# Kernel optimization log

Measured on AMD Instinct MI355X. Metric: run time of the kernel, lower is better.

Reference implementation:

```python
import jax, jax.numpy as jnp
import numpy as np

N = 100000   # nodes
E = 800000   # edges
IN = 128     # in_channels == embedding_size (required by residual Linear)
EMB = 128
OUT = 64
EPS = 1e-5   # GraphNorm eps (PyG default)


def setup_inputs() -> dict:
    key = jax.random.key(0)
    ks = jax.random.split(key, 8)
    x = jax.random.normal(ks[0], (N, IN), jnp.float32)
    edge_index = jax.random.randint(ks[1], (2, E), 0, N, dtype=jnp.int64)
    g = lambda k, shape, scale: jax.random.normal(k, shape, jnp.float32) * scale
    return dict(
        x=x,
        edge_index=edge_index,
        W1=g(ks[2], (IN, EMB), IN ** -0.5), b1=jnp.zeros((EMB,), jnp.float32),
        W2=g(ks[3], (EMB, EMB), EMB ** -0.5), b2=jnp.zeros((EMB,), jnp.float32),
        gn1_w=1.0 + g(ks[4], (EMB,), 0.05), gn1_b=jnp.zeros((EMB,), jnp.float32), gn1_ms=jnp.ones((EMB,), jnp.float32),
        gn2_w=1.0 + g(ks[5], (EMB,), 0.05), gn2_b=jnp.zeros((EMB,), jnp.float32), gn2_ms=jnp.ones((EMB,), jnp.float32),
        Wr=g(ks[6], (EMB, OUT), EMB ** -0.5), br=jnp.zeros((OUT,), jnp.float32),
    )


def _gcn_conv(x, W, b, src, dst, dinv):
    # PyG GCNConv: h = x @ W; out[i] = sum_{(j->i)} dinv[j]*dinv[i]*h[j]; out += bias
    h = x @ W
    norm = (dinv[src] * dinv[dst])[:, None]        # [E+N, 1]
    msg = h[src] * norm                             # gather + scale (irregular)
    out = jax.ops.segment_sum(msg, dst, num_segments=N)  # scatter-add
    return out + b


def _graph_norm(h, w, b, ms):
    # PyG GraphNorm, single graph: mean/var over node dim
    mean = jnp.mean(h, axis=0)
    c = h - ms * mean
    var = jnp.mean(c * c, axis=0)
    return w * c * jax.lax.rsqrt(var + EPS) + b


def reference(x, edge_index, W1, b1, W2, b2, gn1_w, gn1_b, gn1_ms, gn2_w, gn2_b, gn2_ms, Wr, br):
    loops = jnp.arange(N, dtype=edge_index.dtype)
    src = jnp.concatenate([edge_index[0], loops])   # add self-loops
    dst = jnp.concatenate([edge_index[1], loops])
    deg = jax.ops.segment_sum(jnp.ones_like(src, dtype=x.dtype), dst, num_segments=N)
    dinv = jnp.where(deg > 0, jax.lax.rsqrt(jnp.maximum(deg, 1.0)), 0.0)

    # dropout is identity in eval mode
    x1 = jax.nn.relu(_graph_norm(_gcn_conv(x, W1, b1, src, dst, dinv), gn1_w, gn1_b, gn1_ms))
    x2 = jax.nn.relu(_graph_norm(_gcn_conv(x1, W2, b2, src, dst, dinv), gn2_w, gn2_b, gn2_ms))
    return (x1 + x2) @ Wr + br
```

## Files before the change

kernel.cpp:

```cpp
#include <hip/hip_runtime.h>
#include <hip/hip_bf16.h>

typedef __attribute__((ext_vector_type(8))) short bf16x8;
typedef __attribute__((ext_vector_type(4))) float f32x4;
typedef __attribute__((ext_vector_type(2))) float f32x2;
typedef __attribute__((ext_vector_type(4))) unsigned int u32x4;

#define STATS_BLOCKS 256
#define SLOTS 32

__device__ __forceinline__ int coh_load(const int* p){
  return __hip_atomic_load(p, __ATOMIC_RELAXED, __HIP_MEMORY_SCOPE_AGENT);
}
__device__ __forceinline__ unsigned int coh_loadu(const unsigned int* p){
  return __hip_atomic_load(p, __ATOMIC_RELAXED, __HIP_MEMORY_SCOPE_AGENT);
}

__device__ __forceinline__ float bf2f(unsigned short u){
  union { unsigned int i; float f; } v; v.i = ((unsigned int)u) << 16; return v.f;
}
__device__ __forceinline__ unsigned short f2bf(float f){
  union { float f; unsigned int i; } v; v.f = f;
  return (unsigned short)((v.i + 0x7fffu + ((v.i >> 16) & 1u)) >> 16);
}
__device__ __forceinline__ f32x2 bf2x(unsigned int w){
  union { unsigned int i; float f; } lo, hi;
  lo.i = w << 16; hi.i = w & 0xffff0000u;
  f32x2 r; r.x = lo.f; r.y = hi.f; return r;
}


__global__ __launch_bounds__(256) void k_setup(
    const float* __restrict__ W1, const float* __restrict__ W2, const float* __restrict__ Wr,
    unsigned short* __restrict__ wp1, unsigned short* __restrict__ wp2,
    unsigned short* __restrict__ wpr,
    const int* __restrict__ dst, int* __restrict__ hist, int E, int NBUK){
  int b = blockIdx.x;
  if (b < 160){
    int pb = b;
    const float* W; unsigned short* wp; int ncols;
    if (pb < 64)      { W = W1; wp = wp1; ncols = 128; }
    else if (pb < 128){ W = W2; wp = wp2; ncols = 128; pb -= 64; }
    else              { W = Wr; wp = wpr; ncols = 64;  pb -= 128; }
    int idx = pb*256 + threadIdx.x;
    if (idx >= 128*ncols) return;
    int bb = idx & 7, lane = (idx>>3)&63, kk = (idx>>9)&3, ct = idx>>11;
    int k = kk*32 + ((lane>>4)<<3) + bb;
    int c = ct*16 + (lane&15);
    wp[idx] = f2bf(W[k*ncols + c]);
    return;
  }
  int c = b - 160;
  __shared__ int hcnt[256];
  hcnt[threadIdx.x] = 0;
  __syncthreads();
  int per = (E + 255) >> 8;
  int e0 = c*per, e1 = min(E, e0 + per);
  for (int e = e0 + threadIdx.x; e < e1; e += 256)
    atomicAdd(&hcnt[dst[e] >> 9], 1);
  __syncthreads();
  int t = threadIdx.x;
  if (t < NBUK) hist[t*256 + c] = hcnt[t];
}


__global__ __launch_bounds__(256) void k_scanA(int* __restrict__ hist,
                                               int* __restrict__ btot){
  int b = blockIdx.x, t = threadIdx.x;
  int v = hist[b*256 + t];
  __shared__ int sh[256];
  sh[t] = v; __syncthreads();
  for (int o = 1; o < 256; o <<= 1){
    int x = (t >= o) ? sh[t-o] : 0;
    __syncthreads();
    sh[t] += x;
    __syncthreads();
  }
  hist[b*256 + t] = sh[t] - v;
  if (t == 255) btot[b] = sh[255];
}


__global__ __launch_bounds__(256) void k_scanB(const int* __restrict__ btot,
                                               int* __restrict__ bstart, int NBUK){
  int t = threadIdx.x;
  int v = (t < NBUK) ? btot[t] : 0;
  __shared__ int sh[256];
  sh[t] = v; __syncthreads();
  for (int o = 1; o < 256; o <<= 1){
    int x = (t >= o) ? sh[t-o] : 0;
    __syncthreads();
    sh[t] += x;
    __syncthreads();
  }
  if (t < NBUK){
    bstart[t] = sh[t] - v;
    if (t == NBUK-1) bstart[NBUK] = sh[t];
  }
}


__global__ __launch_bounds__(256) void k_scatter(const int* __restrict__ src,
    const int* __restrict__ dst, const int* __restrict__ hist,
    const int* __restrict__ bstart, unsigned int* __restrict__ ebuf, int E, int NBUK){
  __shared__ int cursor[256];
  int c = blockIdx.x, t = threadIdx.x;
  if (t < NBUK) cursor[t] = hist[t*256 + c] + bstart[t];
  __syncthreads();
  int per = (E + 255) >> 8;
  int e0 = c*per, e1 = min(E, e0 + per);
  for (int e = e0 + t; e < e1; e += 256){
    int d = dst[e], s = src[e];
    int bin = d >> 9;
    int pos = atomicAdd(&cursor[bin], 1);
    ebuf[pos] = ((unsigned int)(d & 511) << 17) | (unsigned int)s;
  }
}


__global__ __launch_bounds__(256) void k_bucket(const unsigned int* __restrict__ ebuf,
    const int* __restrict__ bstart, int* __restrict__ cur, int* __restrict__ col, int N){
  __shared__ int cnt[512];
  int b = blockIdx.x, t = threadIdx.x;
  cnt[t] = 0; cnt[t + 256] = 0;
  __syncthreads();
  int e0 = bstart[b], e1 = bstart[b+1];
  int base = b << 9;
  for (int e = e0 + t; e < e1; e += 256){
    unsigned int v = coh_loadu(&ebuf[e]);
    int dl = (int)(v >> 17);
    int s  = (int)(v & 0x1FFFFu);
    int p = atomicAdd(&cnt[dl], 1);
    if (p < SLOTS) col[(size_t)(base + dl)*SLOTS + p] = s;
  }
  __syncthreads();
  int d0 = base + t, d1 = base + t + 256;
  if (d0 < N) cur[d0] = cnt[t];
  if (d1 < N) cur[d1] = cnt[t + 256];
}


__global__ __launch_bounds__(256) void k_gemm1(const float* __restrict__ A,
    const unsigned short* __restrict__ wp, const int* cur,
    unsigned short* __restrict__ h, int nTiles){
  int gw = (int)((blockIdx.x*256 + threadIdx.x) >> 6);
  if (gw >= nTiles) return;
  int lane = threadIdx.x & 63;
  int row0 = gw*16;
  int r  = row0 + (lane & 15);
  int kb = (lane >> 4) * 8;
  bf16x8 a[4];
#pragma unroll
  for (int kk = 0; kk < 4; ++kk){
    const float* p = A + (size_t)r*128 + kk*32 + kb;
    f32x4 v0 = *reinterpret_cast<const f32x4*>(p);
    f32x4 v1 = *reinterpret_cast<const f32x4*>(p + 4);
#pragma unroll
    for (int b = 0; b < 4; ++b){ a[kk][b] = (short)f2bf(v0[b]); a[kk][4+b] = (short)f2bf(v1[b]); }
  }
  int cst = lane & 15;
  int rb  = row0 + ((lane >> 4) << 2);
  float dv[4];
#pragma unroll
  for (int b2 = 0; b2 < 4; ++b2) dv[b2] = rsqrtf(1.0f + (float)coh_load(&cur[rb + b2]));
#pragma unroll
  for (int ct = 0; ct < 8; ++ct){
    f32x4 acc = {0.f,0.f,0.f,0.f};
#pragma unroll
    for (int kk = 0; kk < 4; ++kk){
      bf16x8 b = *reinterpret_cast<const bf16x8*>(wp + ((ct*4 + kk)*64 + lane)*8);
      acc = __builtin_amdgcn_mfma_f32_16x16x32_bf16(a[kk], b, acc, 0, 0, 0);
    }
    int c = ct*16 + cst;
#pragma unroll
    for (int b2 = 0; b2 < 4; ++b2)
      h[(size_t)(rb + b2)*128 + c] = f2bf(dv[b2]*acc[b2]);
  }
}


__global__ __launch_bounds__(256) void k_agg(const unsigned short* __restrict__ h,
    const int* cur, const int* col,
    const float* __restrict__ bias, unsigned short* __restrict__ agg, int N){
  int i = (int)((blockIdx.x*256 + threadIdx.x) >> 6);
  if (i >= N) return;
  int lane = threadIdx.x & 63;
  int q  = lane >> 4;
  int cl = lane & 15;
  const u32x4* hp = reinterpret_cast<const u32x4*>(h);
  int craw = coh_load(&cur[i]);
  int colv = coh_load(&col[i*SLOTS + min(lane, SLOTS-1)]);
  int c = min(craw, SLOTS);
  int idx = (lane < c) ? colv : i;
  f32x2 a0 = {0.f,0.f}, a1 = {0.f,0.f}, a2 = {0.f,0.f}, a3 = {0.f,0.f};
  int j = 0;
  for (; j + 8 <= c; j += 8){
    int r0 = __shfl(idx, j + q);
    int r1 = __shfl(idx, j + 4 + q);
    u32x4 v0 = hp[(size_t)r0*16 + cl];
    u32x4 v1 = hp[(size_t)r1*16 + cl];
    a0 += bf2x(v0.x) + bf2x(v1.x);
    a1 += bf2x(v0.y) + bf2x(v1.y);
    a2 += bf2x(v0.z) + bf2x(v1.z);
    a3 += bf2x(v0.w) + bf2x(v1.w);
  }
  int rem = c - j;
  if (rem > 0){
    int r0 = __shfl(idx, j + q);
    int r1 = __shfl(idx, j + 4 + q);
    if (q < rem){
      u32x4 v0 = hp[(size_t)r0*16 + cl];
      a0 += bf2x(v0.x); a1 += bf2x(v0.y); a2 += bf2x(v0.z); a3 += bf2x(v0.w);
    }
    if (q + 4 < rem){
      u32x4 v1 = hp[(size_t)r1*16 + cl];
      a0 += bf2x(v1.x); a1 += bf2x(v1.y); a2 += bf2x(v1.z); a3 += bf2x(v1.w);
    }
  }
  float acc[8] = {a0.x, a0.y, a1.x, a1.y, a2.x, a2.y, a3.x, a3.y};
#pragma unroll
  for (int b = 0; b < 8; ++b){
    acc[b] += __shfl_xor(acc[b], 16);
    acc[b] += __shfl_xor(acc[b], 32);
  }
  if (q == 0){
    u32x4 hv = hp[(size_t)i*16 + cl];
    float di = rsqrtf(1.0f + (float)craw);
    f32x2 s0 = bf2x(hv.x), s1 = bf2x(hv.y), s2 = bf2x(hv.z), s3 = bf2x(hv.w);
    float sf[8] = {s0.x, s0.y, s1.x, s1.y, s2.x, s2.y, s3.x, s3.y};
    unsigned short o[8];
#pragma unroll
    for (int b = 0; b < 8; ++b)
      o[b] = f2bf(di*(acc[b] + sf[b]) + bias[cl*8 + b]);
    u32x4 ov;
    ov.x = (unsigned int)o[0] | ((unsigned int)o[1] << 16);
    ov.y = (unsigned int)o[2] | ((unsigned int)o[3] << 16);
    ov.z = (unsigned int)o[4] | ((unsigned int)o[5] << 16);
    ov.w = (unsigned int)o[6] | ((unsigned int)o[7] << 16);
    reinterpret_cast<u32x4*>(agg)[(size_t)i*16 + cl] = ov;
  }
}


__global__ __launch_bounds__(256) void k_stats(const unsigned short* __restrict__ agg,
    float* __restrict__ partials, int N){
  int tid = blockIdx.x*256 + threadIdx.x;
  int g = threadIdx.x & 15;
  int c0 = g * 8;
  float S1[8] = {0,0,0,0,0,0,0,0}, S2[8] = {0,0,0,0,0,0,0,0};
  size_t total = (size_t)N * 16;
  for (size_t p = tid; p < total; p += (size_t)STATS_BLOCKS*256){
    bf16x8 v = reinterpret_cast<const bf16x8*>(agg)[p];
#pragma unroll
    for (int b = 0; b < 8; ++b){
      float f = bf2f((unsigned short)v[b]);
      S1[b] += f; S2[b] += f*f;
    }
  }
  __shared__ float sh1[16][128];
  __shared__ float sh2[16][128];
  int cp = threadIdx.x >> 4;
#pragma unroll
  for (int b = 0; b < 8; ++b){ sh1[cp][c0 + b] = S1[b]; sh2[cp][c0 + b] = S2[b]; }
  __syncthreads();
  int t = threadIdx.x;
  if (t < 128){
    float s = 0.f;
#pragma unroll
    for (int qq = 0; qq < 16; ++qq) s += sh1[qq][t];
    partials[blockIdx.x*256 + t] = s;
  } else {
    int cc = t - 128;
    float s = 0.f;
#pragma unroll
    for (int qq = 0; qq < 16; ++qq) s += sh2[qq][cc];
    partials[blockIdx.x*256 + 128 + cc] = s;
  }
}


__global__ void k_reduce(const float* __restrict__ partials, const float* __restrict__ gw_,
    const float* __restrict__ gb_, const float* __restrict__ gms_,
    float* __restrict__ st, int N){
  int t = threadIdx.x;
  float S = 0.f;
#pragma unroll 8
  for (int b = 0; b < STATS_BLOCKS; ++b)
    S += partials[b*256 + t];
  __shared__ float sh[256];
  sh[t] = S;
  __syncthreads();
  if (t >= 128) return;
  int c = t;
  float S1 = sh[c], S2 = sh[128 + c];
  float m  = S1 / (float)N;
  float ms = gms_[c];
  float var = S2/(float)N - 2.f*ms*m*m + ms*ms*m*m;
  float rs = rsqrtf(var + 1e-5f);
  float wv = gw_[c];
  st[c]       = wv * rs;
  st[128 + c] = gb_[c] - wv*rs*ms*m;
}


__global__ __launch_bounds__(256) void k_gemm2(const unsigned short* __restrict__ agg,
    const float* __restrict__ st, const unsigned short* __restrict__ wp,
    const int* cur, unsigned short* __restrict__ h, int nTiles){
  int gw = (int)((blockIdx.x*256 + threadIdx.x) >> 6);
  if (gw >= nTiles) return;
  int lane = threadIdx.x & 63;
  int row0 = gw*16;
  int r  = row0 + (lane & 15);
  int kb = (lane >> 4) * 8;
  bf16x8 a[4];
#pragma unroll
  for (int kk = 0; kk < 4; ++kk){
    int cb = kk*32 + kb;
    bf16x8 v = *reinterpret_cast<const bf16x8*>(agg + (size_t)r*128 + cb);
    f32x4 s0 = *reinterpret_cast<const f32x4*>(st + cb);
    f32x4 s1 = *reinterpret_cast<const f32x4*>(st + cb + 4);
    f32x4 t0 = *reinterpret_cast<const f32x4*>(st + 128 + cb);
    f32x4 t1 = *reinterpret_cast<const f32x4*>(st + 128 + cb + 4);
#pragma unroll
    for (int b = 0; b < 4; ++b){
      a[kk][b]   = (short)f2bf(fmaxf(0.f, s0[b]*bf2f((unsigned short)v[b])   + t0[b]));
      a[kk][4+b] = (short)f2bf(fmaxf(0.f, s1[b]*bf2f((unsigned short)v[4+b]) + t1[b]));
    }
  }
  int cst = lane & 15;
  int rb  = row0 + ((lane >> 4) << 2);
  float dv[4];
#pragma unroll
  for (int b2 = 0; b2 < 4; ++b2) dv[b2] = rsqrtf(1.0f + (float)coh_load(&cur[rb + b2]));
#pragma unroll
  for (int ct = 0; ct < 8; ++ct){
    f32x4 acc = {0.f,0.f,0.f,0.f};
#pragma unroll
    for (int kk = 0; kk < 4; ++kk){
      bf16x8 b = *reinterpret_cast<const bf16x8*>(wp + ((ct*4 + kk)*64 + lane)*8);
      acc = __builtin_amdgcn_mfma_f32_16x16x32_bf16(a[kk], b, acc, 0, 0, 0);
    }
    int c = ct*16 + cst;
#pragma unroll
    for (int b2 = 0; b2 < 4; ++b2)
      h[(size_t)(rb + b2)*128 + c] = f2bf(dv[b2]*acc[b2]);
  }
}


__global__ __launch_bounds__(256) void k_final(const unsigned short* __restrict__ agg1,
    const unsigned short* __restrict__ agg2, const float* __restrict__ st,
    const unsigned short* __restrict__ wp, const float* __restrict__ br,
    float* __restrict__ out, int nTiles){
  int gw = (int)((blockIdx.x*256 + threadIdx.x) >> 6);
  if (gw >= nTiles) return;
  int lane = threadIdx.x & 63;
  int row0 = gw*16;
  int r  = row0 + (lane & 15);
  int kb = (lane >> 4) * 8;
  bf16x8 a[4];
#pragma unroll
  for (int kk = 0; kk < 4; ++kk){
    int cb = kk*32 + kb;
    bf16x8 g1 = *reinterpret_cast<const bf16x8*>(agg1 + (size_t)r*128 + cb);
    bf16x8 g2 = *reinterpret_cast<const bf16x8*>(agg2 + (size_t)r*128 + cb);
#pragma unroll
    for (int b = 0; b < 8; ++b){
      int c = cb + b;
      float x1v = bf2f(f2bf(fmaxf(0.f, st[c]*bf2f((unsigned short)g1[b]) + st[128 + c])));
      float r2  = fmaxf(0.f, st[256 + c]*bf2f((unsigned short)g2[b]) + st[384 + c]);
      a[kk][b] = (short)f2bf(x1v + r2);
    }
  }
  int cst = lane & 15;
  int rb  = row0 + ((lane >> 4) << 2);
#pragma unroll
  for (int ct = 0; ct < 4; ++ct){
    f32x4 acc = {0.f,0.f,0.f,0.f};
#pragma unroll
    for (int kk = 0; kk < 4; ++kk){
      bf16x8 b = *reinterpret_cast<const bf16x8*>(wp + ((ct*4 + kk)*64 + lane)*8);
      acc = __builtin_amdgcn_mfma_f32_16x16x32_bf16(a[kk], b, acc, 0, 0, 0);
    }
    int c = ct*16 + cst;
    float bias = br[c];
#pragma unroll
    for (int b2 = 0; b2 < 4; ++b2)
      out[(size_t)(rb + b2)*64 + c] = acc[b2] + bias;
  }
}


extern "C" void kernel_launch(void* const* d_in, const int* in_sizes, int n_in,
                              void* d_out, int out_size, void* d_ws, size_t ws_size,
                              hipStream_t stream){
  const float* x    = (const float*)d_in[0];
  const int*   ei   = (const int*)d_in[1];
  const float* W1   = (const float*)d_in[2];
  const float* b1   = (const float*)d_in[3];
  const float* W2   = (const float*)d_in[4];
  const float* b2   = (const float*)d_in[5];
  const float* g1w  = (const float*)d_in[6];
  const float* g1b  = (const float*)d_in[7];
  const float* g1ms = (const float*)d_in[8];
  const float* g2w  = (const float*)d_in[9];
  const float* g2b  = (const float*)d_in[10];
  const float* g2ms = (const float*)d_in[11];
  const float* Wr   = (const float*)d_in[12];
  const float* br   = (const float*)d_in[13];
  float* out = (float*)d_out;

  int N = in_sizes[0] / 128;
  int E = in_sizes[1] / 2;
  const int* srcp = ei;
  const int* dstp = ei + E;

  char* w = (char*)d_ws;
  auto alloc = [&](size_t bytes){ char* p = w; w += (bytes + 255) & ~(size_t)255; return p; };
  int*   cur           = (int*)  alloc((size_t)N*4);
  int*   col           = (int*)  alloc((size_t)N*SLOTS*4);
  int*   hist          = (int*)  alloc(256*256*4);
  int*   btot          = (int*)  alloc(257*4);
  int*   bstart        = (int*)  alloc(257*4);
  unsigned int* ebuf   = (unsigned int*)alloc((size_t)E*4);
  float* partials      = (float*)alloc((size_t)STATS_BLOCKS*256*4);
  float* st            = (float*)alloc(4*128*4);
  unsigned short* wp1  = (unsigned short*)alloc(128*128*2);
  unsigned short* wp2  = (unsigned short*)alloc(128*128*2);
  unsigned short* wpr  = (unsigned short*)alloc(128*64*2);
  unsigned short* h    = (unsigned short*)alloc((size_t)N*128*2);
  unsigned short* agg1 = (unsigned short*)alloc((size_t)N*128*2);
  unsigned short* agg2 = (unsigned short*)alloc((size_t)N*128*2);

  int nTiles = N / 16;
  int gemmBlocks = (nTiles + 3) / 4;
  int NBUK = (N + 511) >> 9;
  int aggBlocks = (N*64 + 255)/256;

  k_setup  <<<160 + 256, 256, 0, stream>>>(W1, W2, Wr, wp1, wp2, wpr, dstp, hist, E, NBUK);
  k_scanA  <<<NBUK, 256, 0, stream>>>(hist, btot);
  k_scanB  <<<1, 256, 0, stream>>>(btot, bstart, NBUK);
  k_scatter<<<256, 256, 0, stream>>>(srcp, dstp, hist, bstart, ebuf, E, NBUK);
  k_bucket <<<NBUK, 256, 0, stream>>>(ebuf, bstart, cur, col, N);

  k_gemm1<<<gemmBlocks, 256, 0, stream>>>(x, wp1, cur, h, nTiles);
  k_agg  <<<aggBlocks, 256, 0, stream>>>(h, cur, col, b1, agg1, N);
  k_stats<<<STATS_BLOCKS, 256, 0, stream>>>(agg1, partials, N);
  k_reduce<<<1, 256, 0, stream>>>(partials, g1w, g1b, g1ms, st, N);

  k_gemm2<<<gemmBlocks, 256, 0, stream>>>(agg1, st, wp2, cur, h, nTiles);
  k_agg  <<<aggBlocks, 256, 0, stream>>>(h, cur, col, b2, agg2, N);
  k_stats<<<STATS_BLOCKS, 256, 0, stream>>>(agg2, partials, N);
  k_reduce<<<1, 256, 0, stream>>>(partials, g2w, g2b, g2ms, st + 256, N);

  k_final<<<gemmBlocks, 256, 0, stream>>>(agg1, agg2, st, wpr, br, out, nTiles);
}
```

Baseline: 213.3 us.

## Fold bucket-start scan into scatter/bucket kernels and process two nodes per wave in aggregation

Removes the single-block k_scanB launch: both k_scatter and k_bucket now recompute the prefix sum of bucket totals in shared memory. k_agg is restructured so each 64-lane wave aggregates two destination nodes (32 lanes each), which halves the number of waves launched and cuts idle lanes for low-degree nodes. It also packs the output to bf16 with v_cvt_pk_bf16_f32, loads the bias with vector loads, and replaces coherent atomic loads of cur with plain restrict loads. In exchange, each scatter and bucket block repeats the redundant scan, and gathers per node issue fewer rows per loop iteration.

```diff
diff --git a/kernel.cpp b/kernel.cpp
--- a/kernel.cpp
+++ b/kernel.cpp
@@ -81,11 +81,13 @@
 }
 
 
-__global__ __launch_bounds__(256) void k_scanB(const int* __restrict__ btot,
-                                               int* __restrict__ bstart, int NBUK){
-  int t = threadIdx.x;
+__global__ __launch_bounds__(256) void k_scatter(const int* __restrict__ src,
+    const int* __restrict__ dst, const int* __restrict__ hist,
+    const int* __restrict__ btot, unsigned int* __restrict__ ebuf, int E, int NBUK){
+  __shared__ int sh[256];
+  __shared__ int cursor[256];
+  int c = blockIdx.x, t = threadIdx.x;
   int v = (t < NBUK) ? btot[t] : 0;
-  __shared__ int sh[256];
   sh[t] = v; __syncthreads();
   for (int o = 1; o < 256; o <<= 1){
     int x = (t >= o) ? sh[t-o] : 0;
@@ -93,19 +95,7 @@
     sh[t] += x;
     __syncthreads();
   }
-  if (t < NBUK){
-    bstart[t] = sh[t] - v;
-    if (t == NBUK-1) bstart[NBUK] = sh[t];
-  }
-}
-
-
-__global__ __launch_bounds__(256) void k_scatter(const int* __restrict__ src,
-    const int* __restrict__ dst, const int* __restrict__ hist,
-    const int* __restrict__ bstart, unsigned int* __restrict__ ebuf, int E, int NBUK){
-  __shared__ int cursor[256];
-  int c = blockIdx.x, t = threadIdx.x;
-  if (t < NBUK) cursor[t] = hist[t*256 + c] + bstart[t];
+  if (t < NBUK) cursor[t] = hist[t*256 + c] + (sh[t] - v);
   __syncthreads();
   int per = (E + 255) >> 8;
   int e0 = c*per, e1 = min(E, e0 + per);
@@ -119,17 +109,28 @@
 
 
 __global__ __launch_bounds__(256) void k_bucket(const unsigned int* __restrict__ ebuf,
-    const int* __restrict__ bstart, int* __restrict__ cur, int* __restrict__ col, int N){
+    const int* __restrict__ btot, int* __restrict__ cur, int* __restrict__ col,
+    int N, int NBUK){
+  __shared__ int sh[256];
   __shared__ int cnt[512];
   int b = blockIdx.x, t = threadIdx.x;
+  int v = (t < NBUK) ? btot[t] : 0;
+  sh[t] = v;
   cnt[t] = 0; cnt[t + 256] = 0;
   __syncthreads();
-  int e0 = bstart[b], e1 = bstart[b+1];
+  for (int o = 1; o < 256; o <<= 1){
+    int x = (t >= o) ? sh[t-o] : 0;
+    __syncthreads();
+    sh[t] += x;
+    __syncthreads();
+  }
+  int e1 = sh[b];
+  int e0 = e1 - btot[b];
   int base = b << 9;
   for (int e = e0 + t; e < e1; e += 256){
-    unsigned int v = coh_loadu(&ebuf[e]);
-    int dl = (int)(v >> 17);
-    int s  = (int)(v & 0x1FFFFu);
+    unsigned int w = coh_loadu(&ebuf[e]);
+    int dl = (int)(w >> 17);
+    int s  = (int)(w & 0x1FFFFu);
     int p = atomicAdd(&cnt[dl], 1);
     if (p < SLOTS) col[(size_t)(base + dl)*SLOTS + p] = s;
   }
@@ -141,7 +142,7 @@
 
 
 __global__ __launch_bounds__(256) void k_gemm1(const float* __restrict__ A,
-    const unsigned short* __restrict__ wp, const int* cur,
+    const unsigned short* __restrict__ wp, const int* __restrict__ cur,
     unsigned short* __restrict__ h, int nTiles){
   int gw = (int)((blockIdx.x*256 + threadIdx.x) >> 6);
   if (gw >= nTiles) return;
@@ -162,7 +163,7 @@
   int rb  = row0 + ((lane >> 4) << 2);
   float dv[4];
 #pragma unroll
-  for (int b2 = 0; b2 < 4; ++b2) dv[b2] = rsqrtf(1.0f + (float)coh_load(&cur[rb + b2]));
+  for (int b2 = 0; b2 < 4; ++b2) dv[b2] = rsqrtf(1.0f + (float)cur[rb + b2]);
 #pragma unroll
   for (int ct = 0; ct < 8; ++ct){
     f32x4 acc = {0.f,0.f,0.f,0.f};
@@ -180,23 +181,26 @@
 
 
 __global__ __launch_bounds__(256) void k_agg(const unsigned short* __restrict__ h,
-    const int* cur, const int* col,
+    const int* __restrict__ cur, const int* col,
     const float* __restrict__ bias, unsigned short* __restrict__ agg, int N){
-  int i = (int)((blockIdx.x*256 + threadIdx.x) >> 6);
-  if (i >= N) return;
+  int gw = (int)((blockIdx.x*256 + threadIdx.x) >> 6);
+  if (gw*2 >= N) return;
   int lane = threadIdx.x & 63;
-  int q  = lane >> 4;
+  int i = gw*2 + (lane >> 5);
+  if (i >= N) i = N - 1;
+  int q  = (lane >> 4) & 1;
   int cl = lane & 15;
+  int base = lane & 32;
   const u32x4* hp = reinterpret_cast<const u32x4*>(h);
-  int craw = coh_load(&cur[i]);
-  int colv = coh_load(&col[i*SLOTS + min(lane, SLOTS-1)]);
+  int craw = cur[i];
+  int colv = coh_load(&col[(size_t)i*SLOTS + (lane & 31)]);
   int c = min(craw, SLOTS);
-  int idx = (lane < c) ? colv : i;
+  int idx = ((lane & 31) < c) ? colv : i;
   f32x2 a0 = {0.f,0.f}, a1 = {0.f,0.f}, a2 = {0.f,0.f}, a3 = {0.f,0.f};
   int j = 0;
-  for (; j + 8 <= c; j += 8){
-    int r0 = __shfl(idx, j + q);
-    int r1 = __shfl(idx, j + 4 + q);
+  for (; j + 4 <= c; j += 4){
+    int r0 = __shfl(idx, base + j + q);
+    int r1 = __shfl(idx, base + j + 2 + q);
     u32x4 v0 = hp[(size_t)r0*16 + cl];
     u32x4 v1 = hp[(size_t)r1*16 + cl];
     a0 += bf2x(v0.x) + bf2x(v1.x);
@@ -206,37 +210,38 @@
   }
   int rem = c - j;
   if (rem > 0){
-    int r0 = __shfl(idx, j + q);
-    int r1 = __shfl(idx, j + 4 + q);
+    int r0 = __shfl(idx, base + j + q);
+    int r1 = __shfl(idx, base + j + 2 + q);
     if (q < rem){
       u32x4 v0 = hp[(size_t)r0*16 + cl];
       a0 += bf2x(v0.x); a1 += bf2x(v0.y); a2 += bf2x(v0.z); a3 += bf2x(v0.w);
     }
-    if (q + 4 < rem){
+    if (q + 2 < rem){
       u32x4 v1 = hp[(size_t)r1*16 + cl];
       a0 += bf2x(v1.x); a1 += bf2x(v1.y); a2 += bf2x(v1.z); a3 += bf2x(v1.w);
     }
   }
   float acc[8] = {a0.x, a0.y, a1.x, a1.y, a2.x, a2.y, a3.x, a3.y};
 #pragma unroll
-  for (int b = 0; b < 8; ++b){
+  for (int b = 0; b < 8; ++b)
     acc[b] += __shfl_xor(acc[b], 16);
-    acc[b] += __shfl_xor(acc[b], 32);
-  }
-  if (q == 0){
+  if ((lane & 16) == 0){
     u32x4 hv = hp[(size_t)i*16 + cl];
     float di = rsqrtf(1.0f + (float)craw);
+    f32x4 bb0 = *reinterpret_cast<const f32x4*>(bias + cl*8);
+    f32x4 bb1 = *reinterpret_cast<const f32x4*>(bias + cl*8 + 4);
     f32x2 s0 = bf2x(hv.x), s1 = bf2x(hv.y), s2 = bf2x(hv.z), s3 = bf2x(hv.w);
     float sf[8] = {s0.x, s0.y, s1.x, s1.y, s2.x, s2.y, s3.x, s3.y};
-    unsigned short o[8];
-#pragma unroll
-    for (int b = 0; b < 8; ++b)
-      o[b] = f2bf(di*(acc[b] + sf[b]) + bias[cl*8 + b]);
+    float fin[8];
+#pragma unroll
+    for (int b = 0; b < 4; ++b) fin[b] = di*(acc[b] + sf[b]) + bb0[b];
+#pragma unroll
+    for (int b = 0; b < 4; ++b) fin[4+b] = di*(acc[4+b] + sf[4+b]) + bb1[b];
     u32x4 ov;
-    ov.x = (unsigned int)o[0] | ((unsigned int)o[1] << 16);
-    ov.y = (unsigned int)o[2] | ((unsigned int)o[3] << 16);
-    ov.z = (unsigned int)o[4] | ((unsigned int)o[5] << 16);
-    ov.w = (unsigned int)o[6] | ((unsigned int)o[7] << 16);
+    asm("v_cvt_pk_bf16_f32 %0, %1, %2" : "=v"(ov.x) : "v"(fin[0]), "v"(fin[1]));
+    asm("v_cvt_pk_bf16_f32 %0, %1, %2" : "=v"(ov.y) : "v"(fin[2]), "v"(fin[3]));
+    asm("v_cvt_pk_bf16_f32 %0, %1, %2" : "=v"(ov.z) : "v"(fin[4]), "v"(fin[5]));
+    asm("v_cvt_pk_bf16_f32 %0, %1, %2" : "=v"(ov.w) : "v"(fin[6]), "v"(fin[7]));
     reinterpret_cast<u32x4*>(agg)[(size_t)i*16 + cl] = ov;
   }
 }
@@ -305,7 +310,7 @@
 
 __global__ __launch_bounds__(256) void k_gemm2(const unsigned short* __restrict__ agg,
     const float* __restrict__ st, const unsigned short* __restrict__ wp,
-    const int* cur, unsigned short* __restrict__ h, int nTiles){
+    const int* __restrict__ cur, unsigned short* __restrict__ h, int nTiles){
   int gw = (int)((blockIdx.x*256 + threadIdx.x) >> 6);
   if (gw >= nTiles) return;
   int lane = threadIdx.x & 63;
@@ -331,7 +336,7 @@
   int rb  = row0 + ((lane >> 4) << 2);
   float dv[4];
 #pragma unroll
-  for (int b2 = 0; b2 < 4; ++b2) dv[b2] = rsqrtf(1.0f + (float)coh_load(&cur[rb + b2]));
+  for (int b2 = 0; b2 < 4; ++b2) dv[b2] = rsqrtf(1.0f + (float)cur[rb + b2]);
 #pragma unroll
   for (int ct = 0; ct < 8; ++ct){
     f32x4 acc = {0.f,0.f,0.f,0.f};
@@ -420,8 +425,7 @@
   int*   cur           = (int*)  alloc((size_t)N*4);
   int*   col           = (int*)  alloc((size_t)N*SLOTS*4);
   int*   hist          = (int*)  alloc(256*256*4);
-  int*   btot          = (int*)  alloc(257*4);
-  int*   bstart        = (int*)  alloc(257*4);
+  int*   btot          = (int*)  alloc(256*4);
   unsigned int* ebuf   = (unsigned int*)alloc((size_t)E*4);
   float* partials      = (float*)alloc((size_t)STATS_BLOCKS*256*4);
   float* st            = (float*)alloc(4*128*4);
@@ -435,13 +439,12 @@
   int nTiles = N / 16;
   int gemmBlocks = (nTiles + 3) / 4;
   int NBUK = (N + 511) >> 9;
-  int aggBlocks = (N*64 + 255)/256;
+  int aggBlocks = (N + 7) / 8;
 
   k_setup  <<<160 + 256, 256, 0, stream>>>(W1, W2, Wr, wp1, wp2, wpr, dstp, hist, E, NBUK);
   k_scanA  <<<NBUK, 256, 0, stream>>>(hist, btot);
-  k_scanB  <<<1, 256, 0, stream>>>(btot, bstart, NBUK);
-  k_scatter<<<256, 256, 0, stream>>>(srcp, dstp, hist, bstart, ebuf, E, NBUK);
-  k_bucket <<<NBUK, 256, 0, stream>>>(ebuf, bstart, cur, col, N);
+  k_scatter<<<256, 256, 0, stream>>>(srcp, dstp, hist, btot, ebuf, E, NBUK);
+  k_bucket <<<NBUK, 256, 0, stream>>>(ebuf, btot, cur, col, N, NBUK);
 
   k_gemm1<<<gemmBlocks, 256, 0, stream>>>(x, wp1, cur, h, nTiles);
   k_agg  <<<aggBlocks, 256, 0, stream>>>(h, cur, col, b1, agg1, N);
```

After: 206.2 us, median of 2. 3.3% less time.
